# Kernel optimization log

Hardware: AMD Instinct MI355X
Metric: run time of the kernel (lower is better)

## Reference

```python
import jax, jax.numpy as jnp
import numpy as np

DIM = 768
HEADS = 12
HEAD_DIM = DIM // HEADS


def setup_inputs() -> dict:
    key = jax.random.key(0)
    ks = jax.random.split(key, 5)
    s = 0.02
    return {
        "x": jax.random.normal(ks[0], (2, 4096, DIM), dtype=jnp.float32),
        "w_qkv": jax.random.normal(ks[1], (DIM, 3 * DIM), dtype=jnp.float32) * s,
        "b_qkv": jax.random.normal(ks[2], (3 * DIM,), dtype=jnp.float32) * s,
        "w_proj": jax.random.normal(ks[3], (DIM, DIM), dtype=jnp.float32) * s,
        "b_proj": jax.random.normal(ks[4], (DIM,), dtype=jnp.float32) * s,
    }


def reference(x, w_qkv, b_qkv, w_proj, b_proj):
    B, N, _ = x.shape
    scale = HEAD_DIM ** (-0.5)
    qkv = x @ w_qkv + b_qkv                              # [B, N, 3*DIM]
    q, k, v = jnp.split(qkv, 3, axis=-1)
    # 'b n (h d) -> b h n d'
    def to_heads(t):
        return t.reshape(B, N, HEADS, HEAD_DIM).transpose(0, 2, 1, 3)
    q, k, v = to_heads(q), to_heads(k), to_heads(v)
    attn = jnp.einsum('bhnd,bhmd->bhnm', q, k) * scale   # [B, H, N, N]
    attn = jax.nn.softmax(attn, axis=-1)
    out = jnp.einsum('bhnm,bhmd->bhnd', attn, v)         # [B, H, N, D]
    out = out.transpose(0, 2, 1, 3).reshape(B, N, DIM)   # 'b h n d -> b n (h d)'
    return out @ w_proj + b_proj
```

## Files before the change

### kernel.cpp

```cpp
#include <hip/hip_runtime.h>
#include <hip/hip_bf16.h>
#include <stdint.h>

typedef _Float16 f16x8 __attribute__((ext_vector_type(8)));
typedef _Float16 f16x4 __attribute__((ext_vector_type(4)));
typedef uint32_t u32x2 __attribute__((ext_vector_type(2)));
typedef uint32_t u32x4 __attribute__((ext_vector_type(4)));
typedef float floatx4 __attribute__((ext_vector_type(4)));

#define NSEQ 4096
#define DIMM 768
#define NHEADS 12
#define HD 64

__device__ __forceinline__ void gload_lds16(const void* g, void* l) {
  typedef __attribute__((address_space(1))) const uint32_t GQ;
  typedef __attribute__((address_space(3))) uint32_t LQ;
  __builtin_amdgcn_global_load_lds((GQ*)g, (LQ*)l, 16, 0, 0);
}

__device__ __forceinline__ uint16_t f16_bits(float v) {
  _Float16 h = (_Float16)v;
  return __builtin_bit_cast(uint16_t, h);
}

__device__ __forceinline__ uint32_t pkrtz(float a, float b) {
  return __builtin_bit_cast(uint32_t, __builtin_amdgcn_cvt_pkrtz(a, b));
}

__device__ __forceinline__ int swz(int row, int e) {
  return row * 64 + ((((e >> 3) ^ (row & 7)) << 3) | (e & 7));
}

__global__ __launch_bounds__(256) void convert_f32_f16(
    const float4* __restrict__ src, f16x8* __restrict__ dst, int n8) {
  const int i = blockIdx.x * 256 + threadIdx.x;
  if (i >= n8) return;
  const float4 a = src[2 * i], b = src[2 * i + 1];
  f16x8 o;
  o[0] = (_Float16)a.x; o[1] = (_Float16)a.y; o[2] = (_Float16)a.z; o[3] = (_Float16)a.w;
  o[4] = (_Float16)b.x; o[5] = (_Float16)b.y; o[6] = (_Float16)b.z; o[7] = (_Float16)b.w;
  dst[i] = o;
}

__global__ __launch_bounds__(256) void transpose_w(
    const float* __restrict__ w0, const float* __restrict__ w1,
    uint16_t* __restrict__ d0, uint16_t* __restrict__ d1) {
  __shared__ uint16_t tile[32][33];
  const int z = blockIdx.z;
  if (z && blockIdx.x >= 24) return;
  const float* src = z ? w1 : w0;
  uint16_t* dst = z ? d1 : d0;
  const int C = z ? 768 : 2304;
  const int R = 768;
  const int c0 = blockIdx.x * 32, r0 = blockIdx.y * 32;
  const int tx = threadIdx.x, ty = threadIdx.y;
#pragma unroll
  for (int i = 0; i < 32; i += 8)
    tile[ty + i][tx] = f16_bits(src[(size_t)(r0 + ty + i) * C + (c0 + tx)]);
  __syncthreads();
#pragma unroll
  for (int i = 0; i < 32; i += 8)
    dst[(size_t)(c0 + ty + i) * R + (r0 + tx)] = tile[tx][ty + i];
}

__global__ __launch_bounds__(256) void gemm_bt(
    const _Float16* __restrict__ A, const _Float16* __restrict__ Bt,
    const float* __restrict__ bias, int K, int mode,
    void* __restrict__ o0, _Float16* __restrict__ o1, _Float16* __restrict__ o2) {
  __shared__ __attribute__((aligned(16))) _Float16 As[3][128 * 32];
  __shared__ __attribute__((aligned(16))) _Float16 Bs[3][128 * 32];
  __shared__ float bias_s[128];
  const int tid = threadIdx.x;
  const int wv = tid >> 6;
  const int lane = tid & 63;
  const int quad = lane >> 4, l16 = lane & 15;
  const int wm = (wv >> 1) * 64, wn = (wv & 1) * 64;
  const int m0 = blockIdx.y * 128, n0 = blockIdx.x * 128;

  if (tid < 128) bias_s[tid] = bias[n0 + tid];

  floatx4 acc[4][4];
#pragma unroll
  for (int i = 0; i < 4; ++i)
#pragma unroll
    for (int j = 0; j < 4; ++j) acc[i][j] = (floatx4){0.f, 0.f, 0.f, 0.f};

  const int gr = lane >> 2, gc = (lane & 3) * 8;
  const _Float16* Ag = A + (size_t)(m0 + wv * 32 + gr) * K + gc;
  const _Float16* Bg = Bt + (size_t)(n0 + wv * 32 + gr) * K + gc;
  const size_t K16 = (size_t)16 * K;

  auto STAGE = [&](int buf, int kt) {
    _Float16* As0 = &As[buf][wv * 1024];
    _Float16* Bs0 = &Bs[buf][wv * 1024];
    gload_lds16(Ag + kt, As0);
    gload_lds16(Ag + kt + K16, As0 + 512);
    gload_lds16(Bg + kt, Bs0);
    gload_lds16(Bg + kt + K16, Bs0 + 512);
  };
  auto COMPUTE = [&](int buf) {
    f16x8 af[4], bfr[4];
#pragma unroll
    for (int i = 0; i < 4; ++i)
      af[i] = *(const f16x8*)&As[buf][(wm + i * 16 + l16) * 32 + quad * 8];
#pragma unroll
    for (int j = 0; j < 4; ++j)
      bfr[j] = *(const f16x8*)&Bs[buf][(wn + j * 16 + l16) * 32 + quad * 8];
    __builtin_amdgcn_s_setprio(1);
#pragma unroll
    for (int i = 0; i < 4; ++i)
#pragma unroll
      for (int j = 0; j < 4; ++j)
        acc[i][j] = __builtin_amdgcn_mfma_f32_16x16x32_f16(af[i], bfr[j], acc[i][j], 0, 0, 0);
    __builtin_amdgcn_s_setprio(0);
  };

  STAGE(0, 0);
  STAGE(1, 32);
  const int nt = K >> 5;
  int b0 = 0, b1 = 1, b2 = 2;
#pragma unroll 1
  for (int t = 0; t < nt - 2; ++t) {
    asm volatile("s_waitcnt vmcnt(4)" ::: "memory");
    __builtin_amdgcn_s_barrier();
    STAGE(b2, (t + 2) * 32);
    COMPUTE(b0);
    const int tmp = b0; b0 = b1; b1 = b2; b2 = tmp;
  }
  asm volatile("s_waitcnt vmcnt(4)" ::: "memory");
  __builtin_amdgcn_s_barrier();
  COMPUTE(b0);
  b0 = b1;
  asm volatile("s_waitcnt vmcnt(0)" ::: "memory");
  __builtin_amdgcn_s_barrier();
  COMPUTE(b0);

  if (mode == 0) {
    float* of = (float*)o0;
#pragma unroll
    for (int i = 0; i < 4; ++i)
#pragma unroll
      for (int j = 0; j < 4; ++j) {
        const int col = n0 + wn + j * 16 + l16;
        const float b = bias_s[wn + j * 16 + l16];
        const int mrow = m0 + wm + i * 16 + quad * 4;
#pragma unroll
        for (int r = 0; r < 4; ++r)
          of[(size_t)(mrow + r) * DIMM + col] = acc[i][j][r] + b;
      }
  } else {
    const int sec = n0 / DIMM;
    if (sec < 2) {
      _Float16* dst = (sec == 0) ? (_Float16*)o0 : o1;
      const float sc = (sec == 0) ? 0.18033688011112042f : 1.0f;
#pragma unroll
      for (int i = 0; i < 4; ++i)
#pragma unroll
        for (int j = 0; j < 4; ++j) {
          const int n = n0 + wn + j * 16 + l16;
          const int c = n - sec * DIMM;
          const int h = c >> 6, d = c & 63;
          const float b = bias_s[wn + j * 16 + l16];
          const int mrow = m0 + wm + i * 16 + quad * 4;
#pragma unroll
          for (int r = 0; r < 4; ++r) {
            const int m = mrow + r;
            const int bb = m >> 12, nr = m & 4095;
            dst[(((size_t)(bb * NHEADS + h)) * NSEQ + nr) * HD + d] =
                (_Float16)((acc[i][j][r] + b) * sc);
          }
        }
    } else {
#pragma unroll
      for (int i = 0; i < 4; ++i)
#pragma unroll
        for (int j = 0; j < 4; ++j) {
          const int c = n0 + wn + j * 16 + l16 - 2 * DIMM;
          const int h = c >> 6, d = c & 63;
          const float b = bias_s[wn + j * 16 + l16];
          const int mrow = m0 + wm + i * 16 + quad * 4;
          const int bb = mrow >> 12, nr = mrow & 4095;
          f16x4 v;
#pragma unroll
          for (int r = 0; r < 4; ++r) v[r] = (_Float16)(acc[i][j][r] + b);
          *(f16x4*)&o2[(((size_t)(bb * NHEADS + h)) * HD + d) * NSEQ + nr] = v;
        }
    }
  }
}

__global__ __launch_bounds__(256, 3) void attn(
    const _Float16* __restrict__ Qg, const _Float16* __restrict__ Kg,
    const _Float16* __restrict__ VTg, _Float16* __restrict__ ctx) {
  __shared__ __attribute__((aligned(16))) _Float16 Pt[128 * 64];
  __shared__ __attribute__((aligned(16))) _Float16 Ks[2][64 * 64];
  __shared__ __attribute__((aligned(16))) _Float16 VTs[2][64 * 64];
  const int tid = threadIdx.x;
  const int wv = tid >> 6, lane = tid & 63;
  const int quad = lane >> 4, l16 = lane & 15;
  const int bi = blockIdx.x;
  const int xcd = bi & 7, j = bi >> 3;
  const int bh = xcd * 3 + (j >> 5);
  const int q0 = (j & 31) * 128;
  const int bb = bh / NHEADS, h = bh - bb * NHEADS;
  const _Float16* Qp = Qg + (size_t)bh * NSEQ * HD;
  const _Float16* Kp = Kg + (size_t)bh * NSEQ * HD;
  const _Float16* VTp = VTg + (size_t)bh * HD * NSEQ;

  const int krow = tid >> 3;
  const int kcol = (((tid & 7) ^ ((tid >> 3) & 7)) * 8);

#pragma unroll
  for (int i = 0; i < 4; ++i)
    gload_lds16(Qp + (size_t)(q0 + i * 32 + krow) * HD + kcol, &Pt[(i * 256 + wv * 64) * 8]);
#pragma unroll
  for (int i = 0; i < 2; ++i) {
    gload_lds16(Kp + (size_t)(i * 32 + krow) * HD + kcol, &Ks[0][(i * 256 + wv * 64) * 8]);
    gload_lds16(VTp + (size_t)(i * 32 + krow) * NSEQ + kcol, &VTs[0][(i * 256 + wv * 64) * 8]);
  }
  __syncthreads();

  f16x8 aq[2][2];
#pragma unroll
  for (int it = 0; it < 2; ++it)
#pragma unroll
    for (int ks = 0; ks < 2; ++ks)
      aq[it][ks] = *(const f16x8*)&Pt[swz(wv * 32 + it * 16 + l16, ks * 32 + quad * 8)];

#pragma unroll
  for (int i = 0; i < 2; ++i) {
    gload_lds16(Kp + (size_t)(64 + i * 32 + krow) * HD + kcol, &Ks[1][(i * 256 + wv * 64) * 8]);
    gload_lds16(VTp + (size_t)(i * 32 + krow) * NSEQ + 64 + kcol, &VTs[1][(i * 256 + wv * 64) * 8]);
  }

  floatx4 o[2][4];
  float lp[2] = {0.f, 0.f};
#pragma unroll
  for (int it = 0; it < 2; ++it)
#pragma unroll
    for (int jn = 0; jn < 4; ++jn) o[it][jn] = (floatx4){0.f, 0.f, 0.f, 0.f};

  f16x8 vr[2][4];
  f16x8 ap[2][2];

  auto QKT = [&](const _Float16* bK, floatx4 (&s)[2][4]) {
#pragma unroll
    for (int ks = 0; ks < 2; ++ks) {
#pragma unroll
      for (int im = 0; im < 4; ++im) {
        const f16x8 bk = *(const f16x8*)&bK[swz(im * 16 + l16, ks * 32 + quad * 8)];
        s[0][im] = __builtin_amdgcn_mfma_f32_16x16x32_f16(bk, aq[0][ks], s[0][im], 0, 0, 0);
        s[1][im] = __builtin_amdgcn_mfma_f32_16x16x32_f16(bk, aq[1][ks], s[1][im], 0, 0, 0);
      }
    }
  };
  auto LDVR = [&](const _Float16* bV) {
#pragma unroll
    for (int kk = 0; kk < 2; ++kk)
#pragma unroll
      for (int jn = 0; jn < 4; ++jn)
        vr[kk][jn] = *(const f16x8*)&bV[swz(jn * 16 + l16, kk * 32 + quad * 8)];
  };
  auto SMAX = [&](floatx4 (&s)[2][4]) {
#pragma unroll
    for (int it = 0; it < 2; ++it) {
      uint32_t w[4][2];
#pragma unroll
      for (int im = 0; im < 4; ++im) {
        float p0 = __builtin_amdgcn_exp2f(s[it][im][0]);
        float p1 = __builtin_amdgcn_exp2f(s[it][im][1]);
        float p2 = __builtin_amdgcn_exp2f(s[it][im][2]);
        float p3 = __builtin_amdgcn_exp2f(s[it][im][3]);
        lp[it] += (p0 + p1) + (p2 + p3);
        w[im][0] = pkrtz(p0, p1);
        w[im][1] = pkrtz(p2, p3);
      }
#pragma unroll
      for (int kk = 0; kk < 2; ++kk) {
        uint32_t a = w[2 * kk][0], c = w[2 * kk + 1][0];
        uint32_t b = w[2 * kk][1], d = w[2 * kk + 1][1];
        asm("v_permlane32_swap_b32 %0, %1" : "+v"(a), "+v"(c));
        asm("v_permlane16_swap_b32 %0, %1" : "+v"(a), "+v"(c));
        asm("v_permlane32_swap_b32 %0, %1" : "+v"(b), "+v"(d));
        asm("v_permlane16_swap_b32 %0, %1" : "+v"(b), "+v"(d));
        const u32x4 pk = {a, b, c, d};
        ap[kk][it] = __builtin_bit_cast(f16x8, pk);
      }
    }
  };
  auto PV = [&]() {
#pragma unroll
    for (int kk = 0; kk < 2; ++kk) {
#pragma unroll
      for (int jn = 0; jn < 4; ++jn) {
        o[0][jn] = __builtin_amdgcn_mfma_f32_16x16x32_f16(ap[kk][0], vr[kk][jn], o[0][jn], 0, 0, 0);
        o[1][jn] = __builtin_amdgcn_mfma_f32_16x16x32_f16(ap[kk][1], vr[kk][jn], o[1][jn], 0, 0, 0);
      }
    }
  };

  {
    floatx4 s[2][4];
#pragma unroll
    for (int it = 0; it < 2; ++it)
#pragma unroll
      for (int im = 0; im < 4; ++im) s[it][im] = (floatx4){0.f, 0.f, 0.f, 0.f};
    __builtin_amdgcn_s_setprio(1);
    QKT(Ks[0], s);
    __builtin_amdgcn_s_setprio(0);
    LDVR(VTs[0]);
    SMAX(s);
  }

  auto REGION = [&](const _Float16* bK, const _Float16* bV,
                    _Float16* wK, _Float16* wV, int kvn, bool dodma) {
    __syncthreads();
    if (dodma) {
#pragma unroll
      for (int i = 0; i < 2; ++i) {
        gload_lds16(Kp + (size_t)(kvn + i * 32 + krow) * HD + kcol, &wK[(i * 256 + wv * 64) * 8]);
        gload_lds16(VTp + (size_t)(i * 32 + krow) * NSEQ + kvn + kcol, &wV[(i * 256 + wv * 64) * 8]);
      }
    }
    floatx4 s[2][4];
#pragma unroll
    for (int it = 0; it < 2; ++it)
#pragma unroll
      for (int im = 0; im < 4; ++im) s[it][im] = (floatx4){0.f, 0.f, 0.f, 0.f};
    __builtin_amdgcn_s_setprio(1);
    QKT(bK, s);
    PV();
    __builtin_amdgcn_s_setprio(0);
    LDVR(bV);
    SMAX(s);
  };

#pragma unroll 1
  for (int p = 0; p < 31; ++p) {
    const int t0 = 2 * p + 1;
    REGION(Ks[1], VTs[1], Ks[0], VTs[0], (t0 + 1) * 64, true);
    REGION(Ks[0], VTs[0], Ks[1], VTs[1], (t0 + 2) * 64, true);
  }
  REGION(Ks[1], VTs[1], Ks[0], VTs[0], 0, false);
  PV();

#pragma unroll
  for (int it = 0; it < 2; ++it) {
    lp[it] += __shfl_xor(lp[it], 16);
    lp[it] += __shfl_xor(lp[it], 32);
  }
#pragma unroll
  for (int it = 0; it < 2; ++it)
#pragma unroll
    for (int r = 0; r < 4; ++r) {
      const int q = q0 + wv * 32 + it * 16 + quad * 4 + r;
      const float lq = __shfl(lp[it], (lane & 48) | (quad * 4 + r));
      const float inv = 1.0f / lq;
      _Float16* dst = ctx + (size_t)(bb * NSEQ + q) * DIMM + h * HD;
#pragma unroll
      for (int jn = 0; jn < 4; ++jn)
        dst[jn * 16 + l16] = (_Float16)(o[it][jn][r] * inv);
    }
}

extern "C" void kernel_launch(void* const* d_in, const int* in_sizes, int n_in,
                              void* d_out, int out_size, void* d_ws, size_t ws_size,
                              hipStream_t stream) {
  char* ws = (char*)d_ws;
  _Float16* xc = (_Float16*)ws;      ws += (size_t)8192 * 768 * 2;
  _Float16* wqkvT = (_Float16*)ws;   ws += (size_t)2304 * 768 * 2;
  _Float16* wprojT = (_Float16*)ws;  ws += (size_t)768 * 768 * 2;
  const size_t qkv_elems = (size_t)2 * NHEADS * NSEQ * HD;
  _Float16* Qb = (_Float16*)ws;      ws += qkv_elems * 2;
  _Float16* Kb = (_Float16*)ws;      ws += qkv_elems * 2;
  _Float16* VTb = (_Float16*)ws;     ws += qkv_elems * 2;
  _Float16* ctx = xc;

  const dim3 tb(32, 8, 1);
  const dim3 b256(256, 1, 1);
  hipLaunchKernelGGL(convert_f32_f16, dim3(3072, 1, 1), b256, 0, stream,
                     (const float4*)d_in[0], (f16x8*)xc, 8192 * 768 / 8);
  hipLaunchKernelGGL(transpose_w, dim3(72, 24, 2), tb, 0, stream,
                     (const float*)d_in[1], (const float*)d_in[3],
                     (uint16_t*)wqkvT, (uint16_t*)wprojT);
  hipLaunchKernelGGL(gemm_bt, dim3(18, 64, 1), b256, 0, stream,
                     xc, wqkvT, (const float*)d_in[2], 768, 1, (void*)Qb, Kb, VTb);
  hipLaunchKernelGGL(attn, dim3(768, 1, 1), b256, 0, stream, Qb, Kb, VTb, ctx);
  hipLaunchKernelGGL(gemm_bt, dim3(6, 64, 1), b256, 0, stream,
                     ctx, wprojT, (const float*)d_in[4], 768, 0, d_out,
                     (_Float16*)nullptr, (_Float16*)nullptr);
}
```

Before: 271.3 us.

## Merge prologue kernels and compute softmax row sums with MFMA against ones

The x fp32-to-fp16 conversion and the weight transposes now run in a single prologue launch, with a third grid slice doing a grid-stride conversion. This removes one kernel launch and lets the two jobs overlap. In attention, the per-row softmax denominator is now accumulated by an extra MFMA of the probability tile against a vector of ones, replacing the per-element VALU adds and the final cross-lane shuffles. That adds two MFMAs per PV step in exchange for fewer VALU ops. The sum is now taken over fp16-rounded probabilities, which matches the values used in PV.

```diff
diff --git a/kernel.cpp b/kernel.cpp
--- a/kernel.cpp
+++ b/kernel.cpp
@@ -32,29 +32,31 @@
   return row * 64 + ((((e >> 3) ^ (row & 7)) << 3) | (e & 7));
 }
 
-__global__ __launch_bounds__(256) void convert_f32_f16(
-    const float4* __restrict__ src, f16x8* __restrict__ dst, int n8) {
-  const int i = blockIdx.x * 256 + threadIdx.x;
-  if (i >= n8) return;
-  const float4 a = src[2 * i], b = src[2 * i + 1];
-  f16x8 o;
-  o[0] = (_Float16)a.x; o[1] = (_Float16)a.y; o[2] = (_Float16)a.z; o[3] = (_Float16)a.w;
-  o[4] = (_Float16)b.x; o[5] = (_Float16)b.y; o[6] = (_Float16)b.z; o[7] = (_Float16)b.w;
-  dst[i] = o;
-}
-
-__global__ __launch_bounds__(256) void transpose_w(
+__global__ __launch_bounds__(256) void prologue(
     const float* __restrict__ w0, const float* __restrict__ w1,
-    uint16_t* __restrict__ d0, uint16_t* __restrict__ d1) {
+    uint16_t* __restrict__ d0, uint16_t* __restrict__ d1,
+    const float4* __restrict__ xsrc, f16x8* __restrict__ xdst, int n8) {
+  const int z = blockIdx.z;
+  const int tx = threadIdx.x, ty = threadIdx.y;
+  if (z == 2) {
+    const int nthr = 72 * 24 * 256;
+    int i = (blockIdx.y * 72 + blockIdx.x) * 256 + ty * 32 + tx;
+    for (; i < n8; i += nthr) {
+      const float4 a = xsrc[2 * i], b = xsrc[2 * i + 1];
+      f16x8 o;
+      o[0] = (_Float16)a.x; o[1] = (_Float16)a.y; o[2] = (_Float16)a.z; o[3] = (_Float16)a.w;
+      o[4] = (_Float16)b.x; o[5] = (_Float16)b.y; o[6] = (_Float16)b.z; o[7] = (_Float16)b.w;
+      xdst[i] = o;
+    }
+    return;
+  }
   __shared__ uint16_t tile[32][33];
-  const int z = blockIdx.z;
   if (z && blockIdx.x >= 24) return;
   const float* src = z ? w1 : w0;
   uint16_t* dst = z ? d1 : d0;
   const int C = z ? 768 : 2304;
   const int R = 768;
   const int c0 = blockIdx.x * 32, r0 = blockIdx.y * 32;
-  const int tx = threadIdx.x, ty = threadIdx.y;
 #pragma unroll
   for (int i = 0; i < 32; i += 8)
     tile[ty + i][tx] = f16_bits(src[(size_t)(r0 + ty + i) * C + (c0 + tx)]);
@@ -234,12 +236,18 @@
     gload_lds16(VTp + (size_t)(i * 32 + krow) * NSEQ + 64 + kcol, &VTs[1][(i * 256 + wv * 64) * 8]);
   }
 
+  f16x8 ones;
+#pragma unroll
+  for (int e = 0; e < 8; ++e) ones[e] = (_Float16)1.0f;
+
   floatx4 o[2][4];
-  float lp[2] = {0.f, 0.f};
-#pragma unroll
-  for (int it = 0; it < 2; ++it)
+  floatx4 lacc[2];
+#pragma unroll
+  for (int it = 0; it < 2; ++it) {
+    lacc[it] = (floatx4){0.f, 0.f, 0.f, 0.f};
 #pragma unroll
     for (int jn = 0; jn < 4; ++jn) o[it][jn] = (floatx4){0.f, 0.f, 0.f, 0.f};
+  }
 
   f16x8 vr[2][4];
   f16x8 ap[2][2];
@@ -272,7 +280,6 @@
         float p1 = __builtin_amdgcn_exp2f(s[it][im][1]);
         float p2 = __builtin_amdgcn_exp2f(s[it][im][2]);
         float p3 = __builtin_amdgcn_exp2f(s[it][im][3]);
-        lp[it] += (p0 + p1) + (p2 + p3);
         w[im][0] = pkrtz(p0, p1);
         w[im][1] = pkrtz(p2, p3);
       }
@@ -292,6 +299,8 @@
   auto PV = [&]() {
 #pragma unroll
     for (int kk = 0; kk < 2; ++kk) {
+      lacc[0] = __builtin_amdgcn_mfma_f32_16x16x32_f16(ap[kk][0], ones, lacc[0], 0, 0, 0);
+      lacc[1] = __builtin_amdgcn_mfma_f32_16x16x32_f16(ap[kk][1], ones, lacc[1], 0, 0, 0);
 #pragma unroll
       for (int jn = 0; jn < 4; ++jn) {
         o[0][jn] = __builtin_amdgcn_mfma_f32_16x16x32_f16(ap[kk][0], vr[kk][jn], o[0][jn], 0, 0, 0);
@@ -346,17 +355,11 @@
   PV();
 
 #pragma unroll
-  for (int it = 0; it < 2; ++it) {
-    lp[it] += __shfl_xor(lp[it], 16);
-    lp[it] += __shfl_xor(lp[it], 32);
-  }
-#pragma unroll
   for (int it = 0; it < 2; ++it)
 #pragma unroll
     for (int r = 0; r < 4; ++r) {
       const int q = q0 + wv * 32 + it * 16 + quad * 4 + r;
-      const float lq = __shfl(lp[it], (lane & 48) | (quad * 4 + r));
-      const float inv = 1.0f / lq;
+      const float inv = 1.0f / lacc[it][r];
       _Float16* dst = ctx + (size_t)(bb * NSEQ + q) * DIMM + h * HD;
 #pragma unroll
       for (int jn = 0; jn < 4; ++jn)
@@ -379,11 +382,10 @@
 
   const dim3 tb(32, 8, 1);
   const dim3 b256(256, 1, 1);
-  hipLaunchKernelGGL(convert_f32_f16, dim3(3072, 1, 1), b256, 0, stream,
+  hipLaunchKernelGGL(prologue, dim3(72, 24, 3), tb, 0, stream,
+                     (const float*)d_in[1], (const float*)d_in[3],
+                     (uint16_t*)wqkvT, (uint16_t*)wprojT,
                      (const float4*)d_in[0], (f16x8*)xc, 8192 * 768 / 8);
-  hipLaunchKernelGGL(transpose_w, dim3(72, 24, 2), tb, 0, stream,
-                     (const float*)d_in[1], (const float*)d_in[3],
-                     (uint16_t*)wqkvT, (uint16_t*)wprojT);
   hipLaunchKernelGGL(gemm_bt, dim3(18, 64, 1), b256, 0, stream,
                      xc, wqkvT, (const float*)d_in[2], 768, 1, (void*)Qb, Kb, VTb);
   hipLaunchKernelGGL(attn, dim3(768, 1, 1), b256, 0, stream, Qb, Kb, VTb, ctx);
```

Result: faster. 265.9 us (-2.0%).
